# Performance work log

Measured on AMD Instinct MI355X. Metric: run time of the kernel, lower is better.

Reference implementation:

```python
import jax, jax.numpy as jnp
import numpy as np


def setup_inputs() -> dict:
    key = jax.random.key(0)
    k1, k2 = jax.random.split(key)
    B, S, N, M = 4, 4, 4096, 4096
    output_points = jax.random.normal(k1, (B, S, N, 3), dtype=jnp.float32)
    target_points = jax.random.normal(k2, (B, S, M, 3), dtype=jnp.float32)
    return {"output_points": output_points, "target_points": target_points, "n_samples": 4096}


def reference(output_points, target_points, n_samples):
    # output_points: [B,S,N,3], target_points: [B,S,M,3] (already sampled to n_samples pts)
    x2 = jnp.sum(output_points * output_points, axis=-1)  # [B,S,N]
    y2 = jnp.sum(target_points * target_points, axis=-1)  # [B,S,M]
    xy = jnp.einsum('bsnd,bsmd->bsnm', output_points, target_points)  # [B,S,N,M]
    # squared pairwise distances; clamp tiny negatives from fp error
    d2 = jnp.maximum(x2[..., :, None] + y2[..., None, :] - 2.0 * xy, 0.0)
    dist1 = jnp.min(d2, axis=-1)  # [B,S,N] NN dist output->target (squared)
    dist2 = jnp.min(d2, axis=-2)  # [B,S,M] NN dist target->output (squared)
    # dist_combined per (b,s) = mean(dist1) + mean(dist2); tensor is [S,B]
    chamfer = jnp.mean(dist1, axis=-1) + jnp.mean(dist2, axis=-1)  # [B,S]
    return chamfer.T  # [n_future_steps, batch_size]
```

## Files before the change

### kernel.cpp

```cpp
#include <hip/hip_runtime.h>


constexpr int B = 4, S = 4, NPTS = 4096, PAIRS = B * S;
constexpr int THREADS = 512;
constexpr int QPT = 8;
constexpr int QPB = 64 * QPT;
constexpr int QTILES = NPTS / QPB;
constexpr int SEG = NPTS / 8;

__global__ __launch_bounds__(THREADS, 2)
void chamfer_q8_kernel(const float* __restrict__ out_pts,
                       const float* __restrict__ tgt_pts,
                       float* __restrict__ out) {
  const int t     = threadIdx.x;
  const int l     = t & 63;
  const int wid   = t >> 6;
  const int qtile = blockIdx.x;
  const int pair  = blockIdx.y;
  const int dir   = blockIdx.z;

  const float* qbase = (dir == 0 ? out_pts : tgt_pts) + (size_t)pair * NPTS * 3;
  const float* rbase = (dir == 0 ? tgt_pts : out_pts) + (size_t)pair * NPTS * 3;

  __shared__ float4 sref[NPTS];

  #pragma unroll
  for (int k = 0; k < 8; ++k) {
    const int i = t + k * THREADS;
    const float rx = rbase[3 * i], ry = rbase[3 * i + 1], rz = rbase[3 * i + 2];
    sref[i] = make_float4(rx, ry, rz, -0.5f * (rx * rx + ry * ry + rz * rz));
  }

  float qx[QPT], qy[QPT], qz[QPT];
  #pragma unroll
  for (int j = 0; j < QPT; ++j) {
    const int q = qtile * QPB + j * 64 + l;
    qx[j] = qbase[3 * q];
    qy[j] = qbase[3 * q + 1];
    qz[j] = qbase[3 * q + 2];
  }

  float acc[QPT];
  #pragma unroll
  for (int j = 0; j < QPT; ++j) acc[j] = -3.0e38f;

  __syncthreads();

  const int base = wid * SEG;
  #pragma unroll 4
  for (int r = 0; r < SEG; ++r) {
    const float4 rf = sref[base + r];
    #pragma unroll
    for (int j = 0; j < QPT; ++j) {
      float g = fmaf(qz[j], rf.z, rf.w);
      g = fmaf(qy[j], rf.y, g);
      g = fmaf(qx[j], rf.x, g);
      acc[j] = fmaxf(acc[j], g);
    }
  }

  __syncthreads();
  float* Sf = reinterpret_cast<float*>(sref);

  #pragma unroll
  for (int j = 0; j < QPT; ++j) Sf[wid * QPB + j * 64 + l] = acc[j];
  if (wid == 0) {
    #pragma unroll
    for (int j = 0; j < QPT; ++j)
      Sf[8 * QPB + j * 64 + l] =
          qx[j] * qx[j] + qy[j] * qy[j] + qz[j] * qz[j];
  }
  __syncthreads();

  float g = Sf[t];
  #pragma unroll
  for (int w = 1; w < 8; ++w) g = fmaxf(g, Sf[w * QPB + t]);
  float d = fmaxf(fmaf(-2.0f, g, Sf[8 * QPB + t]), 0.0f);

  #pragma unroll
  for (int off = 1; off < 64; off <<= 1) d += __shfl_xor(d, off, 64);
  __syncthreads();
  if (l == 0) Sf[9 * QPB + wid] = d;
  __syncthreads();
  if (t == 0) {
    float ssum = 0.0f;
    #pragma unroll
    for (int w = 0; w < 8; ++w) ssum += Sf[9 * QPB + w];
    const int b = pair >> 2, s = pair & 3;
    atomicAdd(&out[s * B + b], ssum * (1.0f / NPTS));
  }
}

extern "C" void kernel_launch(void* const* d_in, const int* in_sizes, int n_in,
                              void* d_out, int out_size, void* d_ws, size_t ws_size,
                              hipStream_t stream) {
  const float* out_pts = (const float*)d_in[0];
  const float* tgt_pts = (const float*)d_in[1];
  float* out = (float*)d_out;

  hipMemsetAsync(out, 0, out_size * sizeof(float), stream);
  dim3 grid(QTILES, PAIRS, 2);
  chamfer_q8_kernel<<<grid, THREADS, 0, stream>>>(out_pts, tgt_pts, out);
}
```

Measured before the change: 103.7 us.

## Use packed FP32 FMAs for the distance inner loop and double block size

The inner distance loop now uses inline v_pk_fma_f32 instructions. Each instruction evaluates the partial dot product for two query points at once, against two reference points per iteration. The block grows to 1024 threads so each wave scans half as many reference points, and the squared query norms are now computed in the epilogue from registers rather than staged in shared memory. This is meant to cut VALU issue count in the hot loop and add waves per CU, at the cost of inline-asm fragility and possible register pressure from the higher launch bound.

```diff
diff --git a/kernel.cpp b/kernel.cpp
--- a/kernel.cpp
+++ b/kernel.cpp
@@ -2,16 +2,29 @@
 
 
 constexpr int B = 4, S = 4, NPTS = 4096, PAIRS = B * S;
-constexpr int THREADS = 512;
+constexpr int THREADS = 1024;
+constexpr int WAVES = THREADS / 64;
 constexpr int QPT = 8;
 constexpr int QPB = 64 * QPT;
 constexpr int QTILES = NPTS / QPB;
-constexpr int SEG = NPTS / 8;
+constexpr int SEG = NPTS / WAVES;
 
-__global__ __launch_bounds__(THREADS, 2)
-void chamfer_q8_kernel(const float* __restrict__ out_pts,
-                       const float* __restrict__ tgt_pts,
-                       float* __restrict__ out) {
+typedef float v2f __attribute__((ext_vector_type(2)));
+
+#define PK_FMA_ZW(g, q, rzw)                                              \
+  asm("v_pk_fma_f32 %0, %1, %2, %2 op_sel:[0,0,1] op_sel_hi:[1,0,1]"      \
+      : "=v"(g) : "v"(q), "v"(rzw))
+#define PK_FMA_Y(g, q, rxy)                                               \
+  asm("v_pk_fma_f32 %0, %1, %2, %0 op_sel:[0,1,0] op_sel_hi:[1,1,1]"      \
+      : "+v"(g) : "v"(q), "v"(rxy))
+#define PK_FMA_X(g, q, rxy)                                               \
+  asm("v_pk_fma_f32 %0, %1, %2, %0 op_sel:[0,0,0] op_sel_hi:[1,0,1]"      \
+      : "+v"(g) : "v"(q), "v"(rxy))
+
+__global__ __launch_bounds__(THREADS, 4)
+void chamfer_pk3_kernel(const float* __restrict__ out_pts,
+                        const float* __restrict__ tgt_pts,
+                        float* __restrict__ out) {
   const int t     = threadIdx.x;
   const int l     = t & 63;
   const int wid   = t >> 6;
@@ -25,19 +38,20 @@
   __shared__ float4 sref[NPTS];
 
   #pragma unroll
-  for (int k = 0; k < 8; ++k) {
+  for (int k = 0; k < NPTS / THREADS; ++k) {
     const int i = t + k * THREADS;
     const float rx = rbase[3 * i], ry = rbase[3 * i + 1], rz = rbase[3 * i + 2];
     sref[i] = make_float4(rx, ry, rz, -0.5f * (rx * rx + ry * ry + rz * rz));
   }
 
-  float qx[QPT], qy[QPT], qz[QPT];
+  v2f qx[4], qy[4], qz[4];
   #pragma unroll
-  for (int j = 0; j < QPT; ++j) {
-    const int q = qtile * QPB + j * 64 + l;
-    qx[j] = qbase[3 * q];
-    qy[j] = qbase[3 * q + 1];
-    qz[j] = qbase[3 * q + 2];
+  for (int p = 0; p < 4; ++p) {
+    const int q0 = qtile * QPB + (2 * p) * 64 + l;
+    const int q1 = q0 + 64;
+    qx[p] = v2f{qbase[3 * q0], qbase[3 * q1]};
+    qy[p] = v2f{qbase[3 * q0 + 1], qbase[3 * q1 + 1]};
+    qz[p] = v2f{qbase[3 * q0 + 2], qbase[3 * q1 + 2]};
   }
 
   float acc[QPT];
@@ -47,15 +61,25 @@
   __syncthreads();
 
   const int base = wid * SEG;
-  #pragma unroll 4
-  for (int r = 0; r < SEG; ++r) {
-    const float4 rf = sref[base + r];
+  #pragma unroll 2
+  for (int r = 0; r < SEG; r += 2) {
+    const float4 rf0 = sref[base + r];
+    const float4 rf1 = sref[base + r + 1];
+    v2f rxy0; rxy0.x = rf0.x; rxy0.y = rf0.y;
+    v2f rzw0; rzw0.x = rf0.z; rzw0.y = rf0.w;
+    v2f rxy1; rxy1.x = rf1.x; rxy1.y = rf1.y;
+    v2f rzw1; rzw1.x = rf1.z; rzw1.y = rf1.w;
     #pragma unroll
-    for (int j = 0; j < QPT; ++j) {
-      float g = fmaf(qz[j], rf.z, rf.w);
-      g = fmaf(qy[j], rf.y, g);
-      g = fmaf(qx[j], rf.x, g);
-      acc[j] = fmaxf(acc[j], g);
+    for (int p = 0; p < 4; ++p) {
+      v2f g0, g1;
+      PK_FMA_ZW(g0, qz[p], rzw0);
+      PK_FMA_Y (g0, qy[p], rxy0);
+      PK_FMA_X (g0, qx[p], rxy0);
+      PK_FMA_ZW(g1, qz[p], rzw1);
+      PK_FMA_Y (g1, qy[p], rxy1);
+      PK_FMA_X (g1, qx[p], rxy1);
+      acc[2 * p]     = fmaxf(fmaxf(acc[2 * p], g0.x), g1.x);
+      acc[2 * p + 1] = fmaxf(fmaxf(acc[2 * p + 1], g0.y), g1.y);
     }
   }
 
@@ -64,28 +88,24 @@
 
   #pragma unroll
   for (int j = 0; j < QPT; ++j) Sf[wid * QPB + j * 64 + l] = acc[j];
-  if (wid == 0) {
-    #pragma unroll
-    for (int j = 0; j < QPT; ++j)
-      Sf[8 * QPB + j * 64 + l] =
-          qx[j] * qx[j] + qy[j] * qy[j] + qz[j] * qz[j];
-  }
   __syncthreads();
 
-  float g = Sf[t];
-  #pragma unroll
-  for (int w = 1; w < 8; ++w) g = fmaxf(g, Sf[w * QPB + t]);
-  float d = fmaxf(fmaf(-2.0f, g, Sf[8 * QPB + t]), 0.0f);
-
-  #pragma unroll
-  for (int off = 1; off < 64; off <<= 1) d += __shfl_xor(d, off, 64);
-  __syncthreads();
-  if (l == 0) Sf[9 * QPB + wid] = d;
+  if (t < QPB) {
+    float g = Sf[t];
+    #pragma unroll
+    for (int w = 1; w < WAVES; ++w) g = fmaxf(g, Sf[w * QPB + t]);
+    const int j = t >> 6, p = j >> 1, h = j & 1;
+    const float x2 = qx[p][h] * qx[p][h] + qy[p][h] * qy[p][h] + qz[p][h] * qz[p][h];
+    float d = fmaxf(fmaf(-2.0f, g, x2), 0.0f);
+    #pragma unroll
+    for (int off = 1; off < 64; off <<= 1) d += __shfl_xor(d, off, 64);
+    if (l == 0) Sf[WAVES * QPB + (t >> 6)] = d;
+  }
   __syncthreads();
   if (t == 0) {
     float ssum = 0.0f;
     #pragma unroll
-    for (int w = 0; w < 8; ++w) ssum += Sf[9 * QPB + w];
+    for (int w = 0; w < QPB / 64; ++w) ssum += Sf[WAVES * QPB + w];
     const int b = pair >> 2, s = pair & 3;
     atomicAdd(&out[s * B + b], ssum * (1.0f / NPTS));
   }
@@ -100,5 +120,5 @@
 
   hipMemsetAsync(out, 0, out_size * sizeof(float), stream);
   dim3 grid(QTILES, PAIRS, 2);
-  chamfer_q8_kernel<<<grid, THREADS, 0, stream>>>(out_pts, tgt_pts, out);
+  chamfer_pk3_kernel<<<grid, THREADS, 0, stream>>>(out_pts, tgt_pts, out);
 }
```

After: 98.21 us. 5.3% less time.
